# Performance work log

Hardware: AMD Instinct MI355X
Metric: run time of the kernel (lower is better)

The kernel has to match this reference:

```python
import jax, jax.numpy as jnp
import numpy as np

LENS = 0.5  # rectangular surrogate-gradient half-width
B, C, T, N = 512, 128, 500, 512

@jax.custom_vjp
def spike_fn(u):
    # Heaviside spike with rectangular surrogate gradient (u = mem - Vth)
    return (u > 0.0).astype(u.dtype)

def _spike_fwd(u):
    return spike_fn(u), u

def _spike_bwd(u, g):
    return (g * (jnp.abs(u) < LENS).astype(g.dtype) / (2.0 * LENS),)

spike_fn.defvjp(_spike_fwd, _spike_bwd)

def setup_inputs():
    key = jax.random.key(0)
    ks = jax.random.split(key, 13)
    def lin_w(k, o, i):
        s = 1.0 / np.sqrt(i)
        return jax.random.uniform(k, (o, i), minval=-s, maxval=s, dtype=jnp.float32)
    def lin_b(k, o, i):
        s = 1.0 / np.sqrt(i)
        return jax.random.uniform(k, (o,), minval=-s, maxval=s, dtype=jnp.float32)
    return dict(
        x=jax.random.normal(ks[0], (B, C, T), dtype=jnp.float32),
        W1=lin_w(ks[1], N, C), b1=lin_b(ks[2], N, C),
        W2=lin_w(ks[3], N, N), b2=lin_b(ks[4], N, N),
        Wr2=lin_w(ks[5], N, N), br2=lin_b(ks[6], N, N),
        W3=lin_w(ks[7], N, N), b3=lin_b(ks[8], N, N),
        Wr3=lin_w(ks[9], N, N), br3=lin_b(ks[10], N, N),
        W4=lin_w(ks[11], 2, N), b4=lin_b(ks[12], 2, N),
        Vth1=jnp.full((N,), 1.0, jnp.float32), tau1=jnp.full((N,), 0.5, jnp.float32),
        Vth2=jnp.full((N,), 1.0, jnp.float32), tau2=jnp.full((N,), 0.5, jnp.float32),
        Vth3=jnp.full((N,), 1.0, jnp.float32), tau3=jnp.full((N,), 0.5, jnp.float32),
        tau_out=jnp.full((2,), 0.5, jnp.float32),
    )

def reference(x, W1, b1, W2, b2, Wr2, br2, W3, b3, Wr3, br3, W4, b4,
              Vth1, tau1, Vth2, tau2, Vth3, tau3, tau_out):
    xt = jnp.transpose(x, (2, 0, 1))  # [T, B, C]
    nb = x.shape[0]
    z = lambda d: jnp.zeros((nb, d), x.dtype)
    carry0 = (z(N), z(N), z(N), z(N), z(N), z(N), z(2), z(N), z(N))

    def step(carry, x_t):
        mem1, sp1, mem2, sp2, mem3, sp3, memo, sc1, sc2 = carry
        # layer 1 (NOTE: original code uses frc2 for layer-1 recurrence; kept faithfully)
        i1 = x_t @ W1.T + b1 + (sp1 @ Wr2.T + br2)
        mem1 = tau1 * mem1 * (1.0 - sp1) + i1  # hard-reset LIF
        s1 = spike_fn(mem1 - Vth1)
        # layer 2
        i2 = s1 @ W2.T + b2 + (sp2 @ Wr2.T + br2)
        mem2 = tau2 * mem2 * (1.0 - sp2) + i2
        s2 = spike_fn(mem2 - Vth2)
        # layer 3 (computed as in original; its output does not feed the readout)
        i3 = s2 @ W3.T + b3 + (sp3 @ Wr3.T + br3)
        mem3 = tau3 * mem3 * (1.0 - sp3) + i3
        s3 = spike_fn(mem3 - Vth3)
        # non-spiking leaky-integrator readout on spikes2 (as in original forward)
        memo = tau_out * memo + (s2 @ W4.T + b4)
        return (mem1, s1, mem2, s2, mem3, s3, memo, sc1 + s1, sc2 + s2), memo

    carry, outs = jax.lax.scan(step, carry0, xt)  # outs: [T, B, 2]
    out = jnp.transpose(outs, (1, 2, 0))  # [B, 2, T]
    steps = xt.shape[0]
    return out, (carry[7] / steps, carry[8] / steps)
```

## Files before the change

kernel.cpp:

```cpp
#include <hip/hip_runtime.h>

#pragma clang fp contract(off)

typedef unsigned short u16;
typedef unsigned int u32;
typedef unsigned long long u64;

#define BB 512
#define CC 128
#define TT 500
#define NN 512
#define T_TILE 32

#define TBL_BYTES 1050624ull
#define CHUNK_ROW_BYTES 1048576ull
#define ST_ARR_BYTES 1048576ull
#define PAD_OFF (512u << 11)

__global__ void prep_weights(const float* __restrict__ W2, const float* __restrict__ Wr2,
                             float* __restrict__ Wr2T, float* __restrict__ W2T) {
  int i = blockIdx.x * blockDim.x + threadIdx.x;
  if (i < 513 * 512) {
    int k = i >> 9, n = i & 511;
    Wr2T[i] = (k < NN) ? Wr2[n * NN + k] : 0.0f;
    W2T[i]  = (k < NN) ? W2[n * NN + k] : 0.0f;
  }
}

__global__ void __launch_bounds__(256, 4)
gemm_i1ff(const float* __restrict__ x, const float* __restrict__ W1,
          float* __restrict__ i1ff, int tBeg, int tLen) {
  const int b = blockIdx.x;
  const int tl0 = blockIdx.y * T_TILE;
  const int tid = threadIdx.x;

  __shared__ __align__(16) float xs[CC * T_TILE];
  __shared__ float W1L[NN * 9];

  for (int i = tid; i < CC * T_TILE; i += 256) {
    int c = i >> 5, j = i & 31;
    int tl = tl0 + j;
    xs[c * T_TILE + j] = (tl < tLen) ? x[(b * CC + c) * TT + (tBeg + tl)] : 0.0f;
  }

  float acc[2][T_TILE];
#pragma unroll
  for (int r = 0; r < 2; ++r)
#pragma unroll
    for (int j = 0; j < T_TILE; ++j) acc[r][j] = 0.0f;

  for (int cp = 0; cp < CC / 8; ++cp) {
    __syncthreads();
    for (int i = tid; i < NN * 8; i += 256) {
      int nn = i >> 3, cc = i & 7;
      W1L[nn * 9 + cc] = W1[nn * CC + cp * 8 + cc];
    }
    __syncthreads();
#pragma unroll
    for (int cc = 0; cc < 8; ++cc) {
      const int c = cp * 8 + cc;
      float w0 = W1L[(tid + 0)   * 9 + cc];
      float w1 = W1L[(tid + 256) * 9 + cc];
      const float4* xp = (const float4*)(xs + c * T_TILE);
#pragma unroll
      for (int j4 = 0; j4 < T_TILE / 4; ++j4) {
        float4 xq = xp[j4];
        const int j = j4 * 4;
        acc[0][j + 0] = __builtin_fmaf(xq.x, w0, acc[0][j + 0]);
        acc[1][j + 0] = __builtin_fmaf(xq.x, w1, acc[1][j + 0]);
        acc[0][j + 1] = __builtin_fmaf(xq.y, w0, acc[0][j + 1]);
        acc[1][j + 1] = __builtin_fmaf(xq.y, w1, acc[1][j + 1]);
        acc[0][j + 2] = __builtin_fmaf(xq.z, w0, acc[0][j + 2]);
        acc[1][j + 2] = __builtin_fmaf(xq.z, w1, acc[1][j + 2]);
        acc[0][j + 3] = __builtin_fmaf(xq.w, w0, acc[0][j + 3]);
        acc[1][j + 3] = __builtin_fmaf(xq.w, w1, acc[1][j + 3]);
      }
    }
  }

#pragma unroll
  for (int j = 0; j < T_TILE; ++j) {
    int tl = tl0 + j;
    if (tl < tLen) {
      float* o = i1ff + ((size_t)b * tLen + tl) * NN;
      o[tid + 0]   = acc[0][j];
      o[tid + 256] = acc[1][j];
    }
  }
}

template <int PRE>
__device__ __forceinline__ float sparse_sum_pre(const float* __restrict__ mat,
                                                const u32* list, int cnt, u32 n4) {
  if (cnt <= 0) return 0.0f;
  const char* base = (const char*)mat;
  const int ng = (cnt + 7) >> 3;
  const int npre = ng < PRE ? ng : PRE;
  float buf[PRE * 8];
#pragma unroll
  for (int g = 0; g < PRE; ++g) {
    if (g < npre) {
      uint4 qa = *(const uint4*)(list + g * 8);
      uint4 qb = *(const uint4*)(list + g * 8 + 4);
      buf[g * 8 + 0] = *(const float*)(base + (qa.x + n4));
      buf[g * 8 + 1] = *(const float*)(base + (qa.y + n4));
      buf[g * 8 + 2] = *(const float*)(base + (qa.z + n4));
      buf[g * 8 + 3] = *(const float*)(base + (qa.w + n4));
      buf[g * 8 + 4] = *(const float*)(base + (qb.x + n4));
      buf[g * 8 + 5] = *(const float*)(base + (qb.y + n4));
      buf[g * 8 + 6] = *(const float*)(base + (qb.z + n4));
      buf[g * 8 + 7] = *(const float*)(base + (qb.w + n4));
    }
  }
  float s = 0.0f;
#pragma unroll
  for (int g = 0; g < PRE; ++g) {
    if (g < npre) {
#pragma unroll
      for (int j = 0; j < 8; ++j) s += buf[g * 8 + j];
    }
  }
  for (int i = PRE * 8; i < cnt; i += 8) {
    uint4 qa = *(const uint4*)(list + i);
    uint4 qb = *(const uint4*)(list + i + 4);
    float f0 = *(const float*)(base + (qa.x + n4));
    float f1 = *(const float*)(base + (qa.y + n4));
    float f2 = *(const float*)(base + (qa.z + n4));
    float f3 = *(const float*)(base + (qa.w + n4));
    float f4 = *(const float*)(base + (qb.x + n4));
    float f5 = *(const float*)(base + (qb.y + n4));
    float f6 = *(const float*)(base + (qb.z + n4));
    float f7 = *(const float*)(base + (qb.w + n4));
    s += f0; s += f1; s += f2; s += f3;
    s += f4; s += f5; s += f6; s += f7;
  }
  return s;
}

__device__ __forceinline__ void build_list(const u64* words, int mybit, int wave,
                                           u32 nOff, int n, u32* slot, int* cnt) {
  int tot = 0, base = 0;
#pragma unroll
  for (int j = 0; j < 8; ++j) {
    u64 w = words[j];
    u32 lo = __builtin_amdgcn_readfirstlane((u32)w);
    u32 hi = __builtin_amdgcn_readfirstlane((u32)(w >> 32));
    int pj = __popc(lo) + __popc(hi);
    if (j < wave) base += pj;
    tot += pj;
  }
  if (tot) {
    if (mybit) {
      u64 w = words[wave];
      int below = __builtin_amdgcn_mbcnt_hi((u32)(w >> 32),
                    __builtin_amdgcn_mbcnt_lo((u32)w, 0u));
      slot[base + below] = nOff;
    }
    if (n < 8) slot[tot + n] = PAD_OFF;
  }
  if (n == 0) *cnt = tot;
}

__global__ void __launch_bounds__(512, 2)
recur2(const float* __restrict__ i1ff, const float* __restrict__ Wr2T,
       const float* __restrict__ W2T, const float* __restrict__ W4,
       const float* __restrict__ b1, const float* __restrict__ b2,
       const float* __restrict__ br2, const float* __restrict__ b4,
       const float* __restrict__ Vth1, const float* __restrict__ tau1,
       const float* __restrict__ Vth2, const float* __restrict__ tau2,
       const float* __restrict__ tau_out, float* __restrict__ out,
       float* __restrict__ stM1, float* __restrict__ stM2,
       u32* __restrict__ stSC1, u32* __restrict__ stSC2,
       u64* __restrict__ stW, float* __restrict__ stMemo,
       int tBeg, int tLen, int isFirst, int isLast) {
  const int n = threadIdx.x, b = blockIdx.x;
  const int lane = n & 63, wave = n >> 6;
  const u32 n4 = (u32)(n << 2);
  const u32 nOff = (u32)(n << 11);

  __shared__ u64 wordsA[8], wordsB[8];
  __shared__ __align__(16) u32 listA[2][520];
  __shared__ __align__(16) u32 listB[2][520];
  __shared__ int cA[2], cB[2];

  float mem1, mem2;
  int sc1, sc2;
  float memo0 = 0.0f, memo1 = 0.0f;
  if (isFirst) {
    mem1 = 0.0f; mem2 = 0.0f; sc1 = 0; sc2 = 0;
    if (n < 8) wordsA[n] = 0ull;
    else if (n < 16) wordsB[n - 8] = 0ull;
  } else {
    mem1 = stM1[b * NN + n]; mem2 = stM2[b * NN + n];
    sc1 = (int)stSC1[b * NN + n]; sc2 = (int)stSC2[b * NN + n];
    if (n < 8) wordsA[n] = stW[b * 16 + n];
    else if (n < 16) wordsB[n - 8] = stW[b * 16 + n];
    if (n == 0) { memo0 = stMemo[b * 2]; memo1 = stMemo[b * 2 + 1]; }
  }
  __syncthreads();
  int sp1 = (int)((wordsA[wave] >> lane) & 1ull);
  int sp2 = (int)((wordsB[wave] >> lane) & 1ull);
  build_list(wordsA, sp1, wave, nOff, n, listA[0], &cA[0]);
  build_list(wordsB, sp2, wave, nOff, n, listB[0], &cB[0]);

  const float b1v = b1[n], b2v = b2[n], br2v = br2[n];
  const float t1 = tau1[n], t2 = tau2[n];
  const float v1 = Vth1[n], v2 = Vth2[n];
  const float to0 = tau_out[0], to1 = tau_out[1];
  const float b40 = b4[0], b41 = b4[1];

  const float* ffp = i1ff + (size_t)b * tLen * NN + n;
  float ffcur = ffp[0];

  for (int t = tBeg; t < tBeg + tLen; ++t) {
    const int tt = t - tBeg;
    const int pp = t & 1, qq = pp ^ 1;
    const int ttn = (tt + 1 < tLen) ? tt + 1 : tt;
    float ffnext = ffp[(size_t)ttn * NN];
    __syncthreads();

    float r1 = sparse_sum_pre<6>(Wr2T, listA[pp], cA[pp], n4);
    float u1 = ffcur + b1v;
    float w1s = r1 + br2v;
    float i1 = u1 + w1s;
    float a1m = t1 * mem1;
    a1m = sp1 ? 0.0f : a1m;
    float m1 = a1m + i1;
    mem1 = m1;
    const int s1 = (m1 - v1) > 0.0f ? 1 : 0;
    u64 ba = __ballot(s1 != 0);
    if (lane == 0) wordsA[wave] = ba;
    __syncthreads();

    build_list(wordsA, s1, wave, nOff, n, listA[qq], &cA[qq]);
    __syncthreads();

    float ff = sparse_sum_pre<6>(W2T, listA[qq], cA[qq], n4);
    float u2 = ff + b2v;
    float r2 = sparse_sum_pre<6>(Wr2T, listB[pp], cB[pp], n4);
    float w2s = r2 + br2v;
    float i2 = u2 + w2s;
    float a2m = t2 * mem2;
    a2m = sp2 ? 0.0f : a2m;
    float m2 = a2m + i2;
    mem2 = m2;
    const int s2 = (m2 - v2) > 0.0f ? 1 : 0;
    u64 bb = __ballot(s2 != 0);
    if (lane == 0) wordsB[wave] = bb;
    sp1 = s1; sp2 = s2; sc1 += s1; sc2 += s2;
    ffcur = ffnext;
    __syncthreads();

    build_list(wordsB, s2, wave, nOff, n, listB[qq], &cB[qq]);

    if (n == 0) {
      float a0 = 0.0f, a1 = 0.0f;
#pragma unroll
      for (int w = 0; w < 8; ++w) {
        u64 m = wordsB[w];
        while (m) {
          int k = (w << 6) + __builtin_ctzll(m);
          m &= m - 1ull;
          a0 += W4[k];
          a1 += W4[NN + k];
        }
      }
      float z0 = to0 * memo0;
      float z1 = to1 * memo1;
      memo0 = z0 + (a0 + b40);
      memo1 = z1 + (a1 + b41);
      out[(b * 2 + 0) * TT + t] = memo0;
      out[(b * 2 + 1) * TT + t] = memo1;
    }
  }

  if (isLast) {
    out[BB * 2 * TT + b * NN + n]           = (float)sc1 / 500.0f;
    out[BB * 2 * TT + BB * NN + b * NN + n] = (float)sc2 / 500.0f;
  } else {
    __syncthreads();
    stM1[b * NN + n] = mem1; stM2[b * NN + n] = mem2;
    stSC1[b * NN + n] = (u32)sc1; stSC2[b * NN + n] = (u32)sc2;
    if (n < 8) stW[b * 16 + n] = wordsA[n];
    else if (n < 16) stW[b * 16 + n] = wordsB[n - 8];
    if (n == 0) { stMemo[b * 2] = memo0; stMemo[b * 2 + 1] = memo1; }
  }
}

__global__ void __launch_bounds__(512) __attribute__((amdgpu_waves_per_eu(2, 2)))
recur_fb(const float* __restrict__ x, const float* __restrict__ W1,
         const float* __restrict__ Wr2T, const float* __restrict__ W2T,
         const float* __restrict__ W4,
         const float* __restrict__ b1, const float* __restrict__ b2,
         const float* __restrict__ br2, const float* __restrict__ b4,
         const float* __restrict__ Vth1, const float* __restrict__ tau1,
         const float* __restrict__ Vth2, const float* __restrict__ tau2,
         const float* __restrict__ tau_out, float* __restrict__ out) {
  const int n = threadIdx.x, b = blockIdx.x;
  const int lane = n & 63, wave = n >> 6;
  const u32 n4 = (u32)(n << 2);
  const u32 nOff = (u32)(n << 11);

  __shared__ float xs[CC];
  __shared__ u64 wordsA[8], wordsB[8];
  __shared__ __align__(16) u32 listA[2][520];
  __shared__ __align__(16) u32 listB[2][520];
  __shared__ int cA[2], cB[2];

  float w1r[CC];
  {
    const float4* wp = (const float4*)(W1 + n * CC);
#pragma unroll
    for (int i = 0; i < CC / 4; ++i) {
      float4 q = wp[i];
      w1r[i * 4 + 0] = q.x; w1r[i * 4 + 1] = q.y;
      w1r[i * 4 + 2] = q.z; w1r[i * 4 + 3] = q.w;
    }
  }

  float mem1 = 0.0f, mem2 = 0.0f;
  const float b1v = b1[n], b2v = b2[n], br2v = br2[n];
  const float t1 = tau1[n], t2 = tau2[n];
  const float v1 = Vth1[n], v2 = Vth2[n];
  const float to0 = tau_out[0], to1 = tau_out[1];
  const float b40 = b4[0], b41 = b4[1];
  int sp1 = 0, sp2 = 0, sc1 = 0, sc2 = 0;
  float memo0 = 0.0f, memo1 = 0.0f;

  if (n == 0) { cA[0] = 0; cB[0] = 0; }
  if (n < 8) wordsA[n] = 0ull;
  else if (n < 16) wordsB[n - 8] = 0ull;

  for (int t = 0; t < TT; ++t) {
    const int pp = t & 1, qq = pp ^ 1;
    if (n < CC) xs[n] = x[(b * CC + n) * TT + t];
    __syncthreads();

    float acc = 0.0f;
#pragma unroll
    for (int c = 0; c < CC; ++c) acc = __builtin_fmaf(xs[c], w1r[c], acc);
    float u1 = acc + b1v;
    float r1 = sparse_sum_pre<6>(Wr2T, listA[pp], cA[pp], n4);
    float w1s = r1 + br2v;
    float i1 = u1 + w1s;
    float a1m = t1 * mem1;
    a1m = sp1 ? 0.0f : a1m;
    float m1 = a1m + i1;
    mem1 = m1;
    const int s1 = (m1 - v1) > 0.0f ? 1 : 0;
    u64 ba = __ballot(s1 != 0);
    if (lane == 0) wordsA[wave] = ba;
    __syncthreads();

    build_list(wordsA, s1, wave, nOff, n, listA[qq], &cA[qq]);
    __syncthreads();

    float ff = sparse_sum_pre<6>(W2T, listA[qq], cA[qq], n4);
    float u2 = ff + b2v;
    float r2 = sparse_sum_pre<6>(Wr2T, listB[pp], cB[pp], n4);
    float w2s = r2 + br2v;
    float i2 = u2 + w2s;
    float a2m = t2 * mem2;
    a2m = sp2 ? 0.0f : a2m;
    float m2 = a2m + i2;
    mem2 = m2;
    const int s2 = (m2 - v2) > 0.0f ? 1 : 0;
    u64 bb = __ballot(s2 != 0);
    if (lane == 0) wordsB[wave] = bb;
    sp1 = s1; sp2 = s2; sc1 += s1; sc2 += s2;
    __syncthreads();

    build_list(wordsB, s2, wave, nOff, n, listB[qq], &cB[qq]);

    if (n == 0) {
      float a0 = 0.0f, a1 = 0.0f;
#pragma unroll
      for (int w = 0; w < 8; ++w) {
        u64 m = wordsB[w];
        while (m) {
          int k = (w << 6) + __builtin_ctzll(m);
          m &= m - 1ull;
          a0 += W4[k];
          a1 += W4[NN + k];
        }
      }
      float z0 = to0 * memo0;
      float z1 = to1 * memo1;
      memo0 = z0 + (a0 + b40);
      memo1 = z1 + (a1 + b41);
      out[(b * 2 + 0) * TT + t] = memo0;
      out[(b * 2 + 1) * TT + t] = memo1;
    }
  }

  out[BB * 2 * TT + b * NN + n]           = (float)sc1 / 500.0f;
  out[BB * 2 * TT + BB * NN + b * NN + n] = (float)sc2 / 500.0f;
}

extern "C" void kernel_launch(void* const* d_in, const int* in_sizes, int n_in,
                              void* d_out, int out_size, void* d_ws, size_t ws_size,
                              hipStream_t stream) {
  (void)in_sizes; (void)n_in; (void)out_size;
  const float* x    = (const float*)d_in[0];
  const float* W1   = (const float*)d_in[1];
  const float* b1   = (const float*)d_in[2];
  const float* W2   = (const float*)d_in[3];
  const float* b2   = (const float*)d_in[4];
  const float* Wr2  = (const float*)d_in[5];
  const float* br2  = (const float*)d_in[6];
  const float* W4   = (const float*)d_in[11];
  const float* b4   = (const float*)d_in[12];
  const float* Vth1 = (const float*)d_in[13];
  const float* tau1 = (const float*)d_in[14];
  const float* Vth2 = (const float*)d_in[15];
  const float* tau2 = (const float*)d_in[16];
  const float* tau_out = (const float*)d_in[19];

  char* ws = (char*)d_ws;

  const size_t aux = 2 * TBL_BYTES + 4 * ST_ARR_BYTES + 512ull * 16 * 8 + 512ull * 2 * 4;

  int chunkT = 0;
  if (ws_size > aux) {
    long long ct = (long long)((ws_size - aux) / CHUNK_ROW_BYTES);
    if (ct > TT) ct = TT;
    ct &= ~1LL;
    if (ct >= 16) chunkT = (int)ct;
  }

  if (chunkT >= 16) {
    char* p = ws;
    float* i1ff = (float*)p;  p += (size_t)chunkT * CHUNK_ROW_BYTES;
    float* Wr2T = (float*)p;  p += TBL_BYTES;
    float* W2T  = (float*)p;  p += TBL_BYTES;
    float* stM1 = (float*)p;  p += ST_ARR_BYTES;
    float* stM2 = (float*)p;  p += ST_ARR_BYTES;
    u32* stSC1  = (u32*)p;    p += ST_ARR_BYTES;
    u32* stSC2  = (u32*)p;    p += ST_ARR_BYTES;
    u64* stW    = (u64*)p;    p += 512ull * 16 * 8;
    float* stMemo = (float*)p;

    hipLaunchKernelGGL(prep_weights, dim3((513 * 512 + 255) / 256), dim3(256), 0, stream,
                       W2, Wr2, Wr2T, W2T);
    for (int t0 = 0; t0 < TT; t0 += chunkT) {
      int len = (TT - t0 < chunkT) ? (TT - t0) : chunkT;
      hipLaunchKernelGGL(gemm_i1ff, dim3(BB, (len + T_TILE - 1) / T_TILE), dim3(256), 0,
                         stream, x, W1, i1ff, t0, len);
      hipLaunchKernelGGL(recur2, dim3(BB), dim3(512), 0, stream,
                         i1ff, Wr2T, W2T, W4, b1, b2, br2, b4,
                         Vth1, tau1, Vth2, tau2, tau_out, (float*)d_out,
                         stM1, stM2, stSC1, stSC2, stW, stMemo,
                         t0, len, (t0 == 0) ? 1 : 0, (t0 + len == TT) ? 1 : 0);
    }
  } else {
    float* Wr2T = (float*)ws;
    float* W2T  = (float*)(ws + TBL_BYTES);
    hipLaunchKernelGGL(prep_weights, dim3((513 * 512 + 255) / 256), dim3(256), 0, stream,
                       W2, Wr2, Wr2T, W2T);
    hipLaunchKernelGGL(recur_fb, dim3(BB), dim3(512), 0, stream,
                       x, W1, Wr2T, W2T, W4, b1, b2, br2, b4,
                       Vth1, tau1, Vth2, tau2, tau_out, (float*)d_out);
  }
}
```

Before: 2.713 ms.

## Restructure i1 feedforward GEMM to keep W1 half resident in LDS across time tiles

The input-projection GEMM now launches one 1024-thread block per (batch, 256-neuron half). Each block loads its W1 slice into padded LDS once and loops over all time tiles, instead of reloading W1 in 8-column pieces for every 32-step tile. Each thread computes 8 timesteps for one neuron. This cuts repeated W1 global and LDS traffic and the barriers between pieces. In exchange it uses about 144KB of dynamic LDS per block, so occupancy is lower, and there are fewer blocks per launch.

Result: slower. 2.956 ms (+8.9%).

```diff
diff --git a/kernel.cpp b/kernel.cpp
--- a/kernel.cpp
+++ b/kernel.cpp
@@ -10,12 +10,15 @@
 #define CC 128
 #define TT 500
 #define NN 512
-#define T_TILE 32
+#define GT 32
 
 #define TBL_BYTES 1050624ull
 #define CHUNK_ROW_BYTES 1048576ull
 #define ST_ARR_BYTES 1048576ull
 #define PAD_OFF (512u << 11)
+
+#define W1L_PITCH 257
+#define GEMM_LDS_BYTES (CC * W1L_PITCH * 4 + CC * GT * 4)
 
 __global__ void prep_weights(const float* __restrict__ W2, const float* __restrict__ Wr2,
                              float* __restrict__ Wr2T, float* __restrict__ W2T) {
@@ -27,64 +30,60 @@
   }
 }
 
-__global__ void __launch_bounds__(256, 4)
+__global__ void __launch_bounds__(1024, 4)
 gemm_i1ff(const float* __restrict__ x, const float* __restrict__ W1,
           float* __restrict__ i1ff, int tBeg, int tLen) {
   const int b = blockIdx.x;
-  const int tl0 = blockIdx.y * T_TILE;
+  const int nbase = blockIdx.y * 256;
   const int tid = threadIdx.x;
-
-  __shared__ __align__(16) float xs[CC * T_TILE];
-  __shared__ float W1L[NN * 9];
-
-  for (int i = tid; i < CC * T_TILE; i += 256) {
-    int c = i >> 5, j = i & 31;
-    int tl = tl0 + j;
-    xs[c * T_TILE + j] = (tl < tLen) ? x[(b * CC + c) * TT + (tBeg + tl)] : 0.0f;
-  }
-
-  float acc[2][T_TILE];
-#pragma unroll
-  for (int r = 0; r < 2; ++r)
-#pragma unroll
-    for (int j = 0; j < T_TILE; ++j) acc[r][j] = 0.0f;
-
-  for (int cp = 0; cp < CC / 8; ++cp) {
-    __syncthreads();
-    for (int i = tid; i < NN * 8; i += 256) {
-      int nn = i >> 3, cc = i & 7;
-      W1L[nn * 9 + cc] = W1[nn * CC + cp * 8 + cc];
-    }
-    __syncthreads();
-#pragma unroll
-    for (int cc = 0; cc < 8; ++cc) {
-      const int c = cp * 8 + cc;
-      float w0 = W1L[(tid + 0)   * 9 + cc];
-      float w1 = W1L[(tid + 256) * 9 + cc];
-      const float4* xp = (const float4*)(xs + c * T_TILE);
-#pragma unroll
-      for (int j4 = 0; j4 < T_TILE / 4; ++j4) {
-        float4 xq = xp[j4];
-        const int j = j4 * 4;
-        acc[0][j + 0] = __builtin_fmaf(xq.x, w0, acc[0][j + 0]);
-        acc[1][j + 0] = __builtin_fmaf(xq.x, w1, acc[1][j + 0]);
-        acc[0][j + 1] = __builtin_fmaf(xq.y, w0, acc[0][j + 1]);
-        acc[1][j + 1] = __builtin_fmaf(xq.y, w1, acc[1][j + 1]);
-        acc[0][j + 2] = __builtin_fmaf(xq.z, w0, acc[0][j + 2]);
-        acc[1][j + 2] = __builtin_fmaf(xq.z, w1, acc[1][j + 2]);
-        acc[0][j + 3] = __builtin_fmaf(xq.w, w0, acc[0][j + 3]);
-        acc[1][j + 3] = __builtin_fmaf(xq.w, w1, acc[1][j + 3]);
-      }
-    }
-  }
-
-#pragma unroll
-  for (int j = 0; j < T_TILE; ++j) {
-    int tl = tl0 + j;
-    if (tl < tLen) {
-      float* o = i1ff + ((size_t)b * tLen + tl) * NN;
-      o[tid + 0]   = acc[0][j];
-      o[tid + 256] = acc[1][j];
+  const int n = tid & 255;
+  const int oct = tid >> 8;
+
+  extern __shared__ float smem[];
+  float* W1L = smem;
+  float* xs  = smem + CC * W1L_PITCH;
+
+  for (int k = 0; k < 32; ++k) {
+    int idx = k * 1024 + tid;
+    int nn = idx >> 7, c = idx & 127;
+    W1L[c * W1L_PITCH + nn] = W1[(nbase + nn) * CC + c];
+  }
+
+  const int ntiles = (tLen + GT - 1) / GT;
+  for (int tile = 0; tile < ntiles; ++tile) {
+    const int tl0 = tile * GT;
+    __syncthreads();
+    for (int i = tid; i < CC * GT; i += 1024) {
+      int c = i >> 5, j = i & 31;
+      int tl = tl0 + j;
+      xs[c * GT + j] = (tl < tLen) ? x[(b * CC + c) * TT + (tBeg + tl)] : 0.0f;
+    }
+    __syncthreads();
+
+    float acc[8];
+#pragma unroll
+    for (int j = 0; j < 8; ++j) acc[j] = 0.0f;
+
+#pragma unroll 4
+    for (int c = 0; c < CC; ++c) {
+      float w = W1L[c * W1L_PITCH + n];
+      const float4 xa = *(const float4*)&xs[c * GT + oct * 8];
+      const float4 xb = *(const float4*)&xs[c * GT + oct * 8 + 4];
+      acc[0] = __builtin_fmaf(xa.x, w, acc[0]);
+      acc[1] = __builtin_fmaf(xa.y, w, acc[1]);
+      acc[2] = __builtin_fmaf(xa.z, w, acc[2]);
+      acc[3] = __builtin_fmaf(xa.w, w, acc[3]);
+      acc[4] = __builtin_fmaf(xb.x, w, acc[4]);
+      acc[5] = __builtin_fmaf(xb.y, w, acc[5]);
+      acc[6] = __builtin_fmaf(xb.z, w, acc[6]);
+      acc[7] = __builtin_fmaf(xb.w, w, acc[7]);
+    }
+
+#pragma unroll
+    for (int j = 0; j < 8; ++j) {
+      int tl = tl0 + oct * 8 + j;
+      if (tl < tLen)
+        i1ff[((size_t)b * tLen + tl) * NN + nbase + n] = acc[j];
     }
   }
 }
@@ -444,8 +443,8 @@
                        W2, Wr2, Wr2T, W2T);
     for (int t0 = 0; t0 < TT; t0 += chunkT) {
       int len = (TT - t0 < chunkT) ? (TT - t0) : chunkT;
-      hipLaunchKernelGGL(gemm_i1ff, dim3(BB, (len + T_TILE - 1) / T_TILE), dim3(256), 0,
-                         stream, x, W1, i1ff, t0, len);
+      hipLaunchKernelGGL(gemm_i1ff, dim3(BB, 2), dim3(1024), GEMM_LDS_BYTES, stream,
+                         x, W1, i1ff, t0, len);
       hipLaunchKernelGGL(recur2, dim3(BB), dim3(512), 0, stream,
                          i1ff, Wr2T, W2T, W4, b1, b2, br2, b4,
                          Vth1, tau1, Vth2, tau2, tau_out, (float*)d_out,
```
